# Performance work log

Hardware: AMD Instinct MI355X
Metric: run time of the kernel (lower is better)

The kernel has to match this reference:

```python
import jax, jax.numpy as jnp
import numpy as np

B, L, D = 1, 512, 1280


def setup_inputs() -> dict:
    key = jax.random.key(0)
    k1, k2, k3 = jax.random.split(key, 3)
    prev_result = jax.random.normal(k1, (B, L, D), dtype=jnp.float32)
    # nn.Linear(2*D, 2): store weight as [2D, 2] so forward is x @ W + b
    W = jax.random.normal(k2, (2 * D, 2), dtype=jnp.float32) * (1.0 / np.sqrt(2 * D))
    b = jax.random.normal(k3, (2,), dtype=jnp.float32) * 0.01
    return {"prev_result": prev_result, "W": W, "b": b}


def reference(prev_result, W, b):
    # Dropout is identity at inference. The torch code builds
    # pairwise = cat(x_i * x_j, x_i - x_j) of shape [B,L,L,2D] then applies
    # Linear(2D, 2). We fuse: split W into the prod half Wp and diff half Wd.
    Wp, Wd = W[:D], W[D:]                                   # each [D, 2]
    # (x_i * x_j) @ Wp  -- bilinear contraction, no [B,L,L,2D] intermediate
    prod_term = jnp.einsum('bid,bjd,dk->bijk', prev_result, prev_result, Wp)
    # (x_i - x_j) @ Wd = (x @ Wd)_i - (x @ Wd)_j
    d_proj = prev_result @ Wd                                # [B, L, 2]
    diff_term = d_proj[:, :, None, :] - d_proj[:, None, :, :]
    prediction = prod_term + diff_term + b                   # [B, L, L, 2]
    prediction = (prediction + prediction.transpose(0, 2, 1, 3)) / 2
    return prediction[:, 1:-1, 1:-1]                         # [B, L-2, L-2, 2]
```

## Files before the change

### kernel.cpp

```cpp
#include <hip/hip_runtime.h>
#include <math.h>

#define D_DIM 1280
#define ODIM  510

typedef short bf16x8 __attribute__((ext_vector_type(8)));
typedef float f32x4  __attribute__((ext_vector_type(4)));
typedef unsigned uintx4 __attribute__((ext_vector_type(4)));

__device__ __forceinline__ unsigned pkbf(float a, float b) {
  unsigned ua = __float_as_uint(a), ub = __float_as_uint(b);
  return ((ua + 0x8000u) >> 16) | ((ub + 0x8000u) & 0xffff0000u);
}

union BFU { uintx4 u; bf16x8 h; };

__global__ __launch_bounds__(256, 2) void pcmd_fused(
    const float* __restrict__ X,
    const float* __restrict__ W,
    const float* __restrict__ b,
    float* __restrict__ out)
{
  __shared__ float sR[4][2][16][17];

  const int t = (int)blockIdx.x;
  int bi = (int)((65.0 - sqrt(4225.0 - 8.0 * (double)t)) * 0.5);
  {
    int s0 = bi * 32 - (bi * (bi - 1)) / 2;
    if (t < s0) { --bi; }
    int s1 = (bi + 1) * 32 - ((bi + 1) * bi) / 2;
    if (t >= s1) { ++bi; }
  }
  const int start = bi * 32 - (bi * (bi - 1)) / 2;
  const int bj = bi + (t - start);

  const int tid  = threadIdx.x;
  const int lane = tid & 63;
  const int wv   = tid >> 6;
  const int m    = lane & 15;
  const int quad = lane >> 4;

  const int i_base = 1 + bi * 16;
  const int j_base = 1 + bj * 16;
  int gi = i_base + m; if (gi > 511) gi = 511;
  int gj = j_base + m; if (gj > 511) gj = 511;

  const int k0 = wv * 320;
  const float* pxi = X + (size_t)gi * D_DIM + k0 + quad * 8;
  const float* pxj = X + (size_t)gj * D_DIM + k0 + quad * 8;
  const float* pw  = W + 2 * (k0 + quad * 8);

  float4 rxi[4][2], rxj[4][2], rw[4][4];
  #pragma unroll
  for (int s = 0; s < 4; ++s) {
    rxi[s][0] = *(const float4*)(pxi + s * 32);
    rxi[s][1] = *(const float4*)(pxi + s * 32 + 4);
    rxj[s][0] = *(const float4*)(pxj + s * 32);
    rxj[s][1] = *(const float4*)(pxj + s * 32 + 4);
    rw[s][0]  = *(const float4*)(pw + s * 64);
    rw[s][1]  = *(const float4*)(pw + s * 64 + 4);
    rw[s][2]  = *(const float4*)(pw + s * 64 + 8);
    rw[s][3]  = *(const float4*)(pw + s * 64 + 12);
  }

  f32x4 acc0 = {0.f, 0.f, 0.f, 0.f};
  f32x4 acc1 = {0.f, 0.f, 0.f, 0.f};

  #pragma unroll
  for (int s = 0; s < 10; ++s) {
    const int cur = s & 3;
    float4 xi0 = rxi[cur][0], xi1 = rxi[cur][1];
    float4 xj0 = rxj[cur][0], xj1 = rxj[cur][1];
    float4 w0 = rw[cur][0], w1 = rw[cur][1], w2 = rw[cur][2], w3 = rw[cur][3];
    if (s + 4 < 10) {
      rxi[cur][0] = *(const float4*)(pxi + (s + 4) * 32);
      rxi[cur][1] = *(const float4*)(pxi + (s + 4) * 32 + 4);
      rxj[cur][0] = *(const float4*)(pxj + (s + 4) * 32);
      rxj[cur][1] = *(const float4*)(pxj + (s + 4) * 32 + 4);
      rw[cur][0]  = *(const float4*)(pw + (s + 4) * 64);
      rw[cur][1]  = *(const float4*)(pw + (s + 4) * 64 + 4);
      rw[cur][2]  = *(const float4*)(pw + (s + 4) * 64 + 8);
      rw[cur][3]  = *(const float4*)(pw + (s + 4) * 64 + 12);
    }

    BFU a0, a1, bb;
    a0.u.x = pkbf(xi0.x * w0.x, xi0.y * w0.z);
    a0.u.y = pkbf(xi0.z * w1.x, xi0.w * w1.z);
    a0.u.z = pkbf(xi1.x * w2.x, xi1.y * w2.z);
    a0.u.w = pkbf(xi1.z * w3.x, xi1.w * w3.z);
    a1.u.x = pkbf(xi0.x * w0.y, xi0.y * w0.w);
    a1.u.y = pkbf(xi0.z * w1.y, xi0.w * w1.w);
    a1.u.z = pkbf(xi1.x * w2.y, xi1.y * w2.w);
    a1.u.w = pkbf(xi1.z * w3.y, xi1.w * w3.w);
    bb.u.x = pkbf(xj0.x, xj0.y);
    bb.u.y = pkbf(xj0.z, xj0.w);
    bb.u.z = pkbf(xj1.x, xj1.y);
    bb.u.w = pkbf(xj1.z, xj1.w);

    acc0 = __builtin_amdgcn_mfma_f32_16x16x32_bf16(a0.h, bb.h, acc0, 0, 0, 0);
    acc1 = __builtin_amdgcn_mfma_f32_16x16x32_bf16(a1.h, bb.h, acc1, 0, 0, 0);
  }

  #pragma unroll
  for (int r = 0; r < 4; ++r) {
    sR[wv][0][quad * 4 + r][m] = acc0[r];
    sR[wv][1][quad * 4 + r][m] = acc1[r];
  }
  __syncthreads();

  const float b0 = b[0], b1 = b[1];
  const int il = tid >> 4, jl = tid & 15;

  {
    const int i = i_base + il, j = j_base + jl;
    if (i <= ODIM && j <= ODIM) {
      float2 v;
      v.x = sR[0][0][il][jl] + sR[1][0][il][jl] + sR[2][0][il][jl] + sR[3][0][il][jl] + b0;
      v.y = sR[0][1][il][jl] + sR[1][1][il][jl] + sR[2][1][il][jl] + sR[3][1][il][jl] + b1;
      *(float2*)(out + ((size_t)(i - 1) * ODIM + (j - 1)) * 2) = v;
    }
  }
  if (bi != bj) {
    const int i = j_base + il, j = i_base + jl;
    if (i <= ODIM && j <= ODIM) {
      float2 v;
      v.x = sR[0][0][jl][il] + sR[1][0][jl][il] + sR[2][0][jl][il] + sR[3][0][jl][il] + b0;
      v.y = sR[0][1][jl][il] + sR[1][1][jl][il] + sR[2][1][jl][il] + sR[3][1][jl][il] + b1;
      *(float2*)(out + ((size_t)(i - 1) * ODIM + (j - 1)) * 2) = v;
    }
  }
}

extern "C" void kernel_launch(void* const* d_in, const int* in_sizes, int n_in,
                              void* d_out, int out_size, void* d_ws, size_t ws_size,
                              hipStream_t stream) {
  const float* X = (const float*)d_in[0];
  const float* W = (const float*)d_in[1];
  const float* b = (const float*)d_in[2];
  float* out = (float*)d_out;
  (void)in_sizes; (void)n_in; (void)out_size; (void)d_ws; (void)ws_size;

  hipLaunchKernelGGL(pcmd_fused, dim3(528), dim3(256), 0, stream, X, W, b, out);
}
```

Baseline: 75.00 us.

## Stage X row tiles through shared memory with coalesced loads before MFMA

Replaces the per-lane strided register prefetch of X rows with cooperative coalesced float4 loads of the 32 i/j rows into a per-wave LDS buffer, processed in three K sub-chunks of 128/128/64 columns. MFMA operands are then read from LDS, and W is loaded directly from global each step. The goal is better global coalescing, at the cost of about 67KB of LDS per block, which may cap occupancy, and of losing the software prefetch overlap.

```diff
diff --git a/kernel.cpp b/kernel.cpp
--- a/kernel.cpp
+++ b/kernel.cpp
@@ -6,21 +6,19 @@
 
 typedef short bf16x8 __attribute__((ext_vector_type(8)));
 typedef float f32x4  __attribute__((ext_vector_type(4)));
-typedef unsigned uintx4 __attribute__((ext_vector_type(4)));
 
 __device__ __forceinline__ unsigned pkbf(float a, float b) {
   unsigned ua = __float_as_uint(a), ub = __float_as_uint(b);
   return ((ua + 0x8000u) >> 16) | ((ub + 0x8000u) & 0xffff0000u);
 }
 
-union BFU { uintx4 u; bf16x8 h; };
-
-__global__ __launch_bounds__(256, 2) void pcmd_fused(
+__global__ __launch_bounds__(256, 2) void pcmd_one(
     const float* __restrict__ X,
     const float* __restrict__ W,
     const float* __restrict__ b,
     float* __restrict__ out)
 {
+  __shared__ float sX[4][32][132];
   __shared__ float sR[4][2][16][17];
 
   const int t = (int)blockIdx.x;
@@ -39,66 +37,56 @@
   const int wv   = tid >> 6;
   const int m    = lane & 15;
   const int quad = lane >> 4;
-
-  const int i_base = 1 + bi * 16;
-  const int j_base = 1 + bj * 16;
-  int gi = i_base + m; if (gi > 511) gi = 511;
-  int gj = j_base + m; if (gj > 511) gj = 511;
-
-  const int k0 = wv * 320;
-  const float* pxi = X + (size_t)gi * D_DIM + k0 + quad * 8;
-  const float* pxj = X + (size_t)gj * D_DIM + k0 + quad * 8;
-  const float* pw  = W + 2 * (k0 + quad * 8);
-
-  float4 rxi[4][2], rxj[4][2], rw[4][4];
-  #pragma unroll
-  for (int s = 0; s < 4; ++s) {
-    rxi[s][0] = *(const float4*)(pxi + s * 32);
-    rxi[s][1] = *(const float4*)(pxi + s * 32 + 4);
-    rxj[s][0] = *(const float4*)(pxj + s * 32);
-    rxj[s][1] = *(const float4*)(pxj + s * 32 + 4);
-    rw[s][0]  = *(const float4*)(pw + s * 64);
-    rw[s][1]  = *(const float4*)(pw + s * 64 + 4);
-    rw[s][2]  = *(const float4*)(pw + s * 64 + 8);
-    rw[s][3]  = *(const float4*)(pw + s * 64 + 12);
-  }
+  const int iT = bi * 16, jT = bj * 16;
+  const int kq = wv * 320;
 
   f32x4 acc0 = {0.f, 0.f, 0.f, 0.f};
   f32x4 acc1 = {0.f, 0.f, 0.f, 0.f};
 
-  #pragma unroll
-  for (int s = 0; s < 10; ++s) {
-    const int cur = s & 3;
-    float4 xi0 = rxi[cur][0], xi1 = rxi[cur][1];
-    float4 xj0 = rxj[cur][0], xj1 = rxj[cur][1];
-    float4 w0 = rw[cur][0], w1 = rw[cur][1], w2 = rw[cur][2], w3 = rw[cur][3];
-    if (s + 4 < 10) {
-      rxi[cur][0] = *(const float4*)(pxi + (s + 4) * 32);
-      rxi[cur][1] = *(const float4*)(pxi + (s + 4) * 32 + 4);
-      rxj[cur][0] = *(const float4*)(pxj + (s + 4) * 32);
-      rxj[cur][1] = *(const float4*)(pxj + (s + 4) * 32 + 4);
-      rw[cur][0]  = *(const float4*)(pw + (s + 4) * 64);
-      rw[cur][1]  = *(const float4*)(pw + (s + 4) * 64 + 4);
-      rw[cur][2]  = *(const float4*)(pw + (s + 4) * 64 + 8);
-      rw[cur][3]  = *(const float4*)(pw + (s + 4) * 64 + 12);
+  #pragma unroll 1
+  for (int sub = 0; sub < 3; ++sub) {
+    const int NS    = (sub == 2) ? 64 : 128;
+    const int koff  = sub * 128;
+    const int sh    = (sub == 2) ? 4 : 5;
+    const int msk   = (NS >> 2) - 1;
+    const int iters = NS >> 3;
+
+    #pragma unroll 4
+    for (int it = 0; it < iters; ++it) {
+      const int idx = it * 64 + lane;
+      const int row = idx >> sh;
+      const int c4  = idx & msk;
+      int gr = (row < 16 ? iT + row : jT + row - 16) + 1;
+      if (gr > 511) gr = 511;
+      float4 v = *(const float4*)(X + (size_t)gr * D_DIM + kq + koff + c4 * 4);
+      *(float4*)&sX[wv][row][c4 * 4] = v;
     }
 
-    BFU a0, a1, bb;
-    a0.u.x = pkbf(xi0.x * w0.x, xi0.y * w0.z);
-    a0.u.y = pkbf(xi0.z * w1.x, xi0.w * w1.z);
-    a0.u.z = pkbf(xi1.x * w2.x, xi1.y * w2.z);
-    a0.u.w = pkbf(xi1.z * w3.x, xi1.w * w3.z);
-    a1.u.x = pkbf(xi0.x * w0.y, xi0.y * w0.w);
-    a1.u.y = pkbf(xi0.z * w1.y, xi0.w * w1.w);
-    a1.u.z = pkbf(xi1.x * w2.y, xi1.y * w2.w);
-    a1.u.w = pkbf(xi1.z * w3.y, xi1.w * w3.w);
-    bb.u.x = pkbf(xj0.x, xj0.y);
-    bb.u.y = pkbf(xj0.z, xj0.w);
-    bb.u.z = pkbf(xj1.x, xj1.y);
-    bb.u.w = pkbf(xj1.z, xj1.w);
+    const int steps = NS >> 5;
+    #pragma unroll 2
+    for (int s = 0; s < steps; ++s) {
+      const int col = s * 32 + quad * 8;
+      const float* xi = &sX[wv][m][col];
+      const float* xj = &sX[wv][16 + m][col];
+      float4 xi0 = *(const float4*)xi, xi1 = *(const float4*)(xi + 4);
+      float4 xj0 = *(const float4*)xj, xj1 = *(const float4*)(xj + 4);
+      const float* pw = W + 2 * (kq + koff + col);
+      float4 w0 = *(const float4*)(pw +  0);
+      float4 w1 = *(const float4*)(pw +  4);
+      float4 w2 = *(const float4*)(pw +  8);
+      float4 w3 = *(const float4*)(pw + 12);
 
-    acc0 = __builtin_amdgcn_mfma_f32_16x16x32_bf16(a0.h, bb.h, acc0, 0, 0, 0);
-    acc1 = __builtin_amdgcn_mfma_f32_16x16x32_bf16(a1.h, bb.h, acc1, 0, 0, 0);
+      union { unsigned u[4]; bf16x8 h; } a0, a1, bb;
+      bb.u[0] = pkbf(xj0.x, xj0.y);            bb.u[1] = pkbf(xj0.z, xj0.w);
+      bb.u[2] = pkbf(xj1.x, xj1.y);            bb.u[3] = pkbf(xj1.z, xj1.w);
+      a0.u[0] = pkbf(xi0.x*w0.x, xi0.y*w0.z);  a0.u[1] = pkbf(xi0.z*w1.x, xi0.w*w1.z);
+      a0.u[2] = pkbf(xi1.x*w2.x, xi1.y*w2.z);  a0.u[3] = pkbf(xi1.z*w3.x, xi1.w*w3.z);
+      a1.u[0] = pkbf(xi0.x*w0.y, xi0.y*w0.w);  a1.u[1] = pkbf(xi0.z*w1.y, xi0.w*w1.w);
+      a1.u[2] = pkbf(xi1.x*w2.y, xi1.y*w2.w);  a1.u[3] = pkbf(xi1.z*w3.y, xi1.w*w3.w);
+
+      acc0 = __builtin_amdgcn_mfma_f32_16x16x32_bf16(a0.h, bb.h, acc0, 0, 0, 0);
+      acc1 = __builtin_amdgcn_mfma_f32_16x16x32_bf16(a1.h, bb.h, acc1, 0, 0, 0);
+    }
   }
 
   #pragma unroll
@@ -112,21 +100,21 @@
   const int il = tid >> 4, jl = tid & 15;
 
   {
-    const int i = i_base + il, j = j_base + jl;
-    if (i <= ODIM && j <= ODIM) {
+    const int oi = iT + il, oj = jT + jl;
+    if (oi < ODIM && oj < ODIM) {
       float2 v;
       v.x = sR[0][0][il][jl] + sR[1][0][il][jl] + sR[2][0][il][jl] + sR[3][0][il][jl] + b0;
       v.y = sR[0][1][il][jl] + sR[1][1][il][jl] + sR[2][1][il][jl] + sR[3][1][il][jl] + b1;
-      *(float2*)(out + ((size_t)(i - 1) * ODIM + (j - 1)) * 2) = v;
+      *(float2*)(out + ((size_t)oi * ODIM + oj) * 2) = v;
     }
   }
   if (bi != bj) {
-    const int i = j_base + il, j = i_base + jl;
-    if (i <= ODIM && j <= ODIM) {
+    const int oi = jT + il, oj = iT + jl;
+    if (oi < ODIM && oj < ODIM) {
       float2 v;
       v.x = sR[0][0][jl][il] + sR[1][0][jl][il] + sR[2][0][jl][il] + sR[3][0][jl][il] + b0;
       v.y = sR[0][1][jl][il] + sR[1][1][jl][il] + sR[2][1][jl][il] + sR[3][1][jl][il] + b1;
-      *(float2*)(out + ((size_t)(i - 1) * ODIM + (j - 1)) * 2) = v;
+      *(float2*)(out + ((size_t)oi * ODIM + oj) * 2) = v;
     }
   }
 }
@@ -140,5 +128,5 @@
   float* out = (float*)d_out;
   (void)in_sizes; (void)n_in; (void)out_size; (void)d_ws; (void)ws_size;
 
-  hipLaunchKernelGGL(pcmd_fused, dim3(528), dim3(256), 0, stream, X, W, b, out);
+  hipLaunchKernelGGL(pcmd_one, dim3(528), dim3(256), 0, stream, X, W, b, out);
 }
```

New measurement: 71.89 us. 1.04x faster.
